# Kernel tuning notes

Measured on AMD Instinct MI355X. Metric: run time of the kernel, lower is better.

Reference implementation:

```python
import jax, jax.numpy as jnp
import numpy as np

B, N, K, D, H = 4, 256, 32, 32, 8
NUM_SPATIAL, NUM_EDGES = 512, 1024


def setup_inputs() -> dict:
    key = jax.random.key(0)
    k1, k2, k3, k4, k5 = jax.random.split(key, 5)
    spatial_pos = jax.random.randint(k1, (B, N, N), 0, NUM_SPATIAL, dtype=jnp.int64)
    edge_input = jax.random.randint(k2, (B, N, N, K), 0, NUM_EDGES + 1, dtype=jnp.int64)
    spatial_emb = jax.random.normal(k3, (NUM_SPATIAL, H), dtype=jnp.float32)
    spatial_emb = spatial_emb.at[0].set(0.0)  # padding_idx=0
    edge_feat_emb = jax.random.normal(k4, (NUM_EDGES + 1, D), dtype=jnp.float32)
    edge_feat_emb = edge_feat_emb.at[0].set(0.0)  # padding_idx=0
    edge_pos_emb = jax.random.normal(k5, (K, D * H), dtype=jnp.float32)
    return {"spatial_pos": spatial_pos, "edge_input": edge_input,
            "spatial_emb": spatial_emb, "edge_feat_emb": edge_feat_emb,
            "edge_pos_emb": edge_pos_emb}


def reference(spatial_pos, edge_input, spatial_emb, edge_feat_emb, edge_pos_emb):
    # spatial bias: gather [B,N,N,H] -> [B,H,N,N]
    spatial_bias = jnp.transpose(spatial_emb[spatial_pos], (0, 3, 1, 2))
    # edge feature gather: [B,N,N,K,D]
    edge_feat = edge_feat_emb[edge_input]
    pos_weight = edge_pos_emb.reshape(K, D, H)  # [K,D,H]
    # per-hop projection then mean over valid hops
    terms = jnp.einsum('bnmkd,kdh->bnmkh', edge_feat, pos_weight)  # [B,N,N,K,H]
    mask = (edge_input != 0)
    path_len = jnp.maximum(mask.sum(axis=-1, keepdims=True).astype(terms.dtype), 1.0)  # [B,N,N,1]
    edge_bias = terms.sum(axis=-2) / path_len  # [B,N,N,H]
    edge_bias = jnp.transpose(edge_bias, (0, 3, 1, 2))  # [B,H,N,N]
    return spatial_bias + edge_bias
```

## Files before the change

### kernel.cpp

```cpp
#include <hip/hip_runtime.h>
#include <hip/hip_bf16.h>

#define BB 4
#define NN 256
#define KK 32
#define DD 32
#define HH 8
#define NROWS 1024
#define NPTS (BB * NN * NN)
#define NNSQ (NN * NN)
#define TPB 1024
#define NBLK (NPTS / TPB)
#define NPH 16
#define PK 2
#define SLICE_US (NROWS * HH)

typedef __attribute__((ext_vector_type(8))) unsigned short ushort8;
typedef __attribute__((ext_vector_type(4))) int iv4;

__device__ __forceinline__ unsigned short f2bf(float f) {
    unsigned u = __float_as_uint(f);
    unsigned r = (u + 0x7FFFu + ((u >> 16) & 1u)) >> 16;
    return (unsigned short)r;
}

__global__ __launch_bounds__(256) void build_proj_bf16(
    const float* __restrict__ feat,
    const float* __restrict__ w,
    unsigned short* __restrict__ proj)
{
    int t  = blockIdx.x * 256 + threadIdx.x;
    int k  = t >> 10;
    int e  = (t & 1023) + 1;

    const float* frow = feat + (size_t)e * DD;
    const float* wrow = w + (size_t)k * DD * HH;

    float acc[HH];
#pragma unroll
    for (int h = 0; h < HH; ++h) acc[h] = 0.0f;

#pragma unroll
    for (int d = 0; d < DD; ++d) {
        float f = frow[d];
#pragma unroll
        for (int h = 0; h < HH; ++h) acc[h] = fmaf(f, wrow[d * HH + h], acc[h]);
    }

    ushort8 o;
#pragma unroll
    for (int h = 0; h < HH; ++h) o[h] = f2bf(acc[h]);
    *(ushort8*)(proj + (size_t)t * HH) = o;
}

template <int E>
__global__ __launch_bounds__(TPB) void attn_bias_v5(
    const int* __restrict__ sp,
    const int* __restrict__ ei,
    const float* __restrict__ semb,
    const unsigned short* __restrict__ proj,
    float* __restrict__ out)
{
    __shared__ __align__(16) unsigned short tbuf[2][PK * SLICE_US];
    __shared__ unsigned short ibuf[KK][TPB + 2];

    const int tid = threadIdx.x;
    const int p0  = blockIdx.x * TPB;

    const float4* P4 = (const float4*)proj;

    float4 ra = P4[tid];
    float4 rb = P4[1024 + tid];

    const iv4* EI4 = (const iv4*)ei;
    const size_t base4 = (size_t)p0 * (8 * E);
    if (E == 2) {
#pragma unroll 4
        for (int c = 0; c < 16; ++c) {
            int j  = c * TPB + tid;
            int pt = j >> 4;
            int q  = j & 15;
            iv4 v  = EI4[base4 + (size_t)pt * 16 + q];
            ibuf[2 * q    ][pt] = (unsigned short)v.x;
            ibuf[2 * q + 1][pt] = (unsigned short)v.z;
        }
    } else {
#pragma unroll 4
        for (int c = 0; c < 8; ++c) {
            int j  = c * TPB + tid;
            int pt = j >> 3;
            int q  = j & 7;
            iv4 v  = EI4[base4 + (size_t)pt * 8 + q];
            ibuf[4 * q    ][pt] = (unsigned short)v.x;
            ibuf[4 * q + 1][pt] = (unsigned short)v.y;
            ibuf[4 * q + 2][pt] = (unsigned short)v.z;
            ibuf[4 * q + 3][pt] = (unsigned short)v.w;
        }
    }

    *(float4*)&tbuf[0][tid * 8]        = ra;
    *(float4*)&tbuf[0][SLICE_US + tid * 8] = rb;
    ra = P4[2048 + tid];
    rb = P4[2048 + 1024 + tid];

    __syncthreads();

    float acc[HH];
#pragma unroll
    for (int h = 0; h < HH; ++h) acc[h] = 0.0f;
    int cnt = 0;

#pragma unroll 1
    for (int p = 0; p < NPH; ++p) {
        const unsigned short* tb = tbuf[p & 1];

        int e0 = ibuf[2 * p    ][tid];
        int e1 = ibuf[2 * p + 1][tid];
        int r0 = e0 ? (e0 - 1) : 0;
        int r1 = e1 ? (e1 - 1) : 0;
        float m0 = e0 ? 1.0f : 0.0f;
        float m1 = e1 ? 1.0f : 0.0f;
        cnt += (e0 != 0) + (e1 != 0);

        ushort8 w0 = *(const ushort8*)&tb[r0 * 8];
        ushort8 w1 = *(const ushort8*)&tb[SLICE_US + r1 * 8];
#pragma unroll
        for (int h = 0; h < HH; ++h) {
            acc[h] = fmaf(m0, __uint_as_float(((unsigned)w0[h]) << 16), acc[h]);
            acc[h] = fmaf(m1, __uint_as_float(((unsigned)w1[h]) << 16), acc[h]);
        }

        if (p < NPH - 1) {
            __syncthreads();
            unsigned short* wb = tbuf[(p + 1) & 1];
            *(float4*)&wb[tid * 8]        = ra;
            *(float4*)&wb[SLICE_US + tid * 8] = rb;
            if (p < NPH - 2) {
                ra = P4[(size_t)(p + 2) * 2048 + tid];
                rb = P4[(size_t)(p + 2) * 2048 + 1024 + tid];
            }
            __syncthreads();
        }
    }

    const int p = p0 + tid;
    int s;
    if (E == 2) s = (int)((const long long*)sp)[p];
    else        s = sp[p];
    const float4* srow = (const float4*)(semb + (size_t)s * HH);
    float4 s0 = srow[0], s1 = srow[1];
    float sb[HH] = {s0.x, s0.y, s0.z, s0.w, s1.x, s1.y, s1.z, s1.w};

    float inv = 1.0f / (float)(cnt ? cnt : 1);
    float* o = out + (size_t)(p >> 16) * (HH * NNSQ) + (p & (NNSQ - 1));
#pragma unroll
    for (int h = 0; h < HH; ++h)
        o[(size_t)h * NNSQ] = sb[h] + acc[h] * inv;
}

extern "C" void kernel_launch(void* const* d_in, const int* in_sizes, int n_in,
                              void* d_out, int out_size, void* d_ws, size_t ws_size,
                              hipStream_t stream) {
    const int*   sp = (const int*)d_in[0];
    const int*   ei = (const int*)d_in[1];
    const float* se = (const float*)d_in[2];
    const float* fe = (const float*)d_in[3];
    const float* pw = (const float*)d_in[4];
    float* out = (float*)d_out;

    const bool i64 = (in_sizes[0] == 2 * NPTS);
    unsigned short* proj = (unsigned short*)d_ws;

    build_proj_bf16<<<128, 256, 0, stream>>>(fe, pw, proj);

    if (i64) attn_bias_v5<2><<<NBLK, TPB, 0, stream>>>(sp, ei, se, proj, out);
    else     attn_bias_v5<1><<<NBLK, TPB, 0, stream>>>(sp, ei, se, proj, out);
}
```

Measured before the change: 27.04 us.

## Pipeline edge-index loads in groups and use a single barrier per phase

Edge-index staging into shared memory becomes a double-buffered stream of four groups, each holding eight hops, interleaved with the projection-table phases, rather than one up-front bulk load of all 32 hops. Each pair of hop indices is packed into one 32-bit LDS word, and the two __syncthreads per phase become an lgkmcnt wait plus a single raw s_barrier. The spatial index load is hoisted to the start of the kernel. The goal is to overlap the large edge_input read with compute and cut barrier overhead, at the cost of more register-held prefetch state and a more delicate ordering of LDS writes against the barrier.

```diff
diff --git a/kernel.cpp b/kernel.cpp
--- a/kernel.cpp
+++ b/kernel.cpp
@@ -12,11 +12,15 @@
 #define TPB 1024
 #define NBLK (NPTS / TPB)
 #define NPH 16
-#define PK 2
 #define SLICE_US (NROWS * HH)
+#define IPAD 4
 
 typedef __attribute__((ext_vector_type(8))) unsigned short ushort8;
 typedef __attribute__((ext_vector_type(4))) int iv4;
+typedef __attribute__((ext_vector_type(4))) float fv4;
+
+#define LGKM0 asm volatile("s_waitcnt lgkmcnt(0)" ::: "memory")
+#define BAR   __builtin_amdgcn_s_barrier()
 
 __device__ __forceinline__ unsigned short f2bf(float f) {
     unsigned u = __float_as_uint(f);
@@ -54,56 +58,81 @@
 }
 
 template <int E>
-__global__ __launch_bounds__(TPB) void attn_bias_v5(
+__global__ __launch_bounds__(TPB) void attn_bias_v6(
     const int* __restrict__ sp,
     const int* __restrict__ ei,
     const float* __restrict__ semb,
     const unsigned short* __restrict__ proj,
     float* __restrict__ out)
 {
-    __shared__ __align__(16) unsigned short tbuf[2][PK * SLICE_US];
-    __shared__ unsigned short ibuf[KK][TPB + 2];
+    __shared__ __align__(16) unsigned short tbuf[2][2 * SLICE_US];
+    __shared__ unsigned int ibuf[2][4][NROWS + IPAD];
 
     const int tid = threadIdx.x;
     const int p0  = blockIdx.x * TPB;
 
-    const float4* P4 = (const float4*)proj;
-
-    float4 ra = P4[tid];
-    float4 rb = P4[1024 + tid];
-
+    const fv4* P4  = (const fv4*)proj;
     const iv4* EI4 = (const iv4*)ei;
-    const size_t base4 = (size_t)p0 * (8 * E);
-    if (E == 2) {
-#pragma unroll 4
-        for (int c = 0; c < 16; ++c) {
-            int j  = c * TPB + tid;
-            int pt = j >> 4;
-            int q  = j & 15;
-            iv4 v  = EI4[base4 + (size_t)pt * 16 + q];
-            ibuf[2 * q    ][pt] = (unsigned short)v.x;
-            ibuf[2 * q + 1][pt] = (unsigned short)v.z;
-        }
-    } else {
-#pragma unroll 4
-        for (int c = 0; c < 8; ++c) {
-            int j  = c * TPB + tid;
-            int pt = j >> 3;
-            int q  = j & 7;
-            iv4 v  = EI4[base4 + (size_t)pt * 8 + q];
-            ibuf[4 * q    ][pt] = (unsigned short)v.x;
-            ibuf[4 * q + 1][pt] = (unsigned short)v.y;
-            ibuf[4 * q + 2][pt] = (unsigned short)v.z;
-            ibuf[4 * q + 3][pt] = (unsigned short)v.w;
-        }
-    }
-
-    *(float4*)&tbuf[0][tid * 8]        = ra;
-    *(float4*)&tbuf[0][SLICE_US + tid * 8] = rb;
-    ra = P4[2048 + tid];
-    rb = P4[2048 + 1024 + tid];
-
-    __syncthreads();
+    const size_t bi4 = (size_t)p0 * (8 * E);
+
+    fv4 S0, S1;
+    iv4 cv[4];
+
+    auto issueS = [&](int ph) {
+        S0 = P4[(size_t)(2 * ph)     * 1024 + tid];
+        S1 = P4[(size_t)(2 * ph + 1) * 1024 + tid];
+    };
+    auto writeS = [&](int nb) {
+        *(fv4*)&tbuf[nb][tid * 8]            = S0;
+        *(fv4*)&tbuf[nb][SLICE_US + tid * 8] = S1;
+    };
+    auto issueC = [&](int g) {
+        if (E == 2) {
+#pragma unroll
+            for (int c = 0; c < 4; ++c) {
+                int j = c * TPB + tid, pt = j >> 2, q = j & 3;
+                cv[c] = EI4[bi4 + (size_t)pt * 16 + 4 * g + q];
+            }
+        } else {
+#pragma unroll
+            for (int c = 0; c < 2; ++c) {
+                int j = c * TPB + tid, pt = j >> 1, q = j & 1;
+                cv[c] = EI4[bi4 + (size_t)pt * 8 + 2 * g + q];
+            }
+        }
+    };
+    auto writeC = [&](int nb) {
+        if (E == 2) {
+#pragma unroll
+            for (int c = 0; c < 4; ++c) {
+                int j = c * TPB + tid, pt = j >> 2, q = j & 3;
+                unsigned pk = ((unsigned)cv[c].x & 0xffffu) |
+                              (((unsigned)cv[c].z & 0xffffu) << 16);
+                ibuf[nb][q][pt] = pk;
+            }
+        } else {
+#pragma unroll
+            for (int c = 0; c < 2; ++c) {
+                int j = c * TPB + tid, pt = j >> 1, q = j & 1;
+                ibuf[nb][q * 2][pt] = ((unsigned)cv[c].x & 0xffffu) |
+                                      (((unsigned)cv[c].y & 0xffffu) << 16);
+                ibuf[nb][q * 2 + 1][pt] = ((unsigned)cv[c].z & 0xffffu) |
+                                          (((unsigned)cv[c].w & 0xffffu) << 16);
+            }
+        }
+    };
+
+    issueS(0);
+    issueC(0);
+    const int pg = p0 + tid;
+    int s = (E == 2) ? (int)((const long long*)sp)[pg] : sp[pg];
+
+    writeS(0);
+    issueS(1);
+    writeC(0);
+    issueC(1);
+    LGKM0;
+    BAR;
 
     float acc[HH];
 #pragma unroll
@@ -111,17 +140,19 @@
     int cnt = 0;
 
 #pragma unroll 1
-    for (int p = 0; p < NPH; ++p) {
-        const unsigned short* tb = tbuf[p & 1];
-
-        int e0 = ibuf[2 * p    ][tid];
-        int e1 = ibuf[2 * p + 1][tid];
+    for (int ph = 0; ph < NPH; ++ph) {
+        const int g = ph >> 2;
+
+        unsigned pr = ibuf[g & 1][ph & 3][tid];
+        int e0 = pr & 0xffffu;
+        int e1 = pr >> 16;
         int r0 = e0 ? (e0 - 1) : 0;
         int r1 = e1 ? (e1 - 1) : 0;
         float m0 = e0 ? 1.0f : 0.0f;
         float m1 = e1 ? 1.0f : 0.0f;
         cnt += (e0 != 0) + (e1 != 0);
 
+        const unsigned short* tb = tbuf[ph & 1];
         ushort8 w0 = *(const ushort8*)&tb[r0 * 8];
         ushort8 w1 = *(const ushort8*)&tb[SLICE_US + r1 * 8];
 #pragma unroll
@@ -130,29 +161,24 @@
             acc[h] = fmaf(m1, __uint_as_float(((unsigned)w1[h]) << 16), acc[h]);
         }
 
-        if (p < NPH - 1) {
-            __syncthreads();
-            unsigned short* wb = tbuf[(p + 1) & 1];
-            *(float4*)&wb[tid * 8]        = ra;
-            *(float4*)&wb[SLICE_US + tid * 8] = rb;
-            if (p < NPH - 2) {
-                ra = P4[(size_t)(p + 2) * 2048 + tid];
-                rb = P4[(size_t)(p + 2) * 2048 + 1024 + tid];
-            }
-            __syncthreads();
+        if (ph < NPH - 1) {
+            writeS((ph + 1) & 1);
+            if (ph < NPH - 2) issueS(ph + 2);
+            if ((ph & 3) == 3 && ph < 12) {
+                writeC((g + 1) & 1);
+                if (ph < 8) issueC(g + 2);
+            }
+            LGKM0;
+            BAR;
         }
     }
 
-    const int p = p0 + tid;
-    int s;
-    if (E == 2) s = (int)((const long long*)sp)[p];
-    else        s = sp[p];
     const float4* srow = (const float4*)(semb + (size_t)s * HH);
-    float4 s0 = srow[0], s1 = srow[1];
-    float sb[HH] = {s0.x, s0.y, s0.z, s0.w, s1.x, s1.y, s1.z, s1.w};
+    float4 s0v = srow[0], s1v = srow[1];
+    float sb[HH] = {s0v.x, s0v.y, s0v.z, s0v.w, s1v.x, s1v.y, s1v.z, s1v.w};
 
     float inv = 1.0f / (float)(cnt ? cnt : 1);
-    float* o = out + (size_t)(p >> 16) * (HH * NNSQ) + (p & (NNSQ - 1));
+    float* o = out + (size_t)(pg >> 16) * (HH * NNSQ) + (pg & (NNSQ - 1));
 #pragma unroll
     for (int h = 0; h < HH; ++h)
         o[(size_t)h * NNSQ] = sb[h] + acc[h] * inv;
@@ -173,6 +199,6 @@
 
     build_proj_bf16<<<128, 256, 0, stream>>>(fe, pw, proj);
 
-    if (i64) attn_bias_v5<2><<<NBLK, TPB, 0, stream>>>(sp, ei, se, proj, out);
-    else     attn_bias_v5<1><<<NBLK, TPB, 0, stream>>>(sp, ei, se, proj, out);
-}
+    if (i64) attn_bias_v6<2><<<NBLK, TPB, 0, stream>>>(sp, ei, se, proj, out);
+    else     attn_bias_v6<1><<<NBLK, TPB, 0, stream>>>(sp, ei, se, proj, out);
+}
```

Result: no change. 27.50 us (+1.7%).
